# Performance work log

Measured on AMD Instinct MI355X. Metric: run time of the kernel, lower is better.

Reference implementation:

```python
import jax, jax.numpy as jnp
import numpy as np
import math

LS = [0, 1, 2]            # degrees present in all irreps
MAX_L = 2
MULT_IN = 64
MULT_MID = 16
MULT_OUT = 64
N = 20000

# ---- Clebsch-Gordan coefficients in the real spherical-harmonic basis ----

def _f(n):
    return math.factorial(int(n))

def _cg_complex(j1, m1, j2, m2, j3, m3):
    if m1 + m2 != m3:
        return 0.0
    pre = math.sqrt((2 * j3 + 1) * _f(j1 + j2 - j3) * _f(j1 - j2 + j3) * _f(-j1 + j2 + j3) / _f(j1 + j2 + j3 + 1))
    pre *= math.sqrt(_f(j1 + m1) * _f(j1 - m1) * _f(j2 + m2) * _f(j2 - m2) * _f(j3 + m3) * _f(j3 - m3))
    kmin = max(0, j2 - j3 - m1, j1 - j3 + m2)
    kmax = min(j1 + j2 - j3, j1 - m1, j2 + m2)
    s = 0.0
    for k in range(kmin, kmax + 1):
        s += (-1) ** k / (_f(k) * _f(j1 + j2 - j3 - k) * _f(j1 - m1 - k) * _f(j2 + m2 - k) * _f(j3 - j2 + m1 + k) * _f(j3 - j1 - m2 + k))
    return pre * s

def _q(l):
    # complex->real change of basis, rows indexed by real m = -l..l
    Q = np.zeros((2 * l + 1, 2 * l + 1), dtype=complex)
    Q[l, l] = 1.0
    r2 = math.sqrt(2.0)
    for m in range(1, l + 1):
        Q[l + m, l + m] = (-1) ** m / r2
        Q[l + m, l - m] = 1.0 / r2
        Q[l - m, l - m] = 1j / r2
        Q[l - m, l + m] = -1j * (-1) ** m / r2
    return Q

def _real_cg(l1, l2, l3):
    C = np.zeros((2 * l1 + 1, 2 * l2 + 1, 2 * l3 + 1), dtype=complex)
    for m1 in range(-l1, l1 + 1):
        for m2 in range(-l2, l2 + 1):
            m3 = m1 + m2
            if -l3 <= m3 <= l3:
                C[l1 + m1, l2 + m2, l3 + m3] = _cg_complex(l1, m1, l2, m2, l3, m3)
    Q1, Q2, Q3 = _q(l1), _q(l2), _q(l3)
    M = np.einsum('ia,jb,kc,abc->ijk', Q1.conj(), Q2.conj(), Q3, C)
    if np.abs(M.imag).max() > np.abs(M.real).max():
        M = M * (-1j)  # fix parity phase so coefficients are real
    assert np.abs(M.imag).max() < 1e-10
    return np.asarray(M.real, dtype=np.float32)

# triangle-rule paths, truncated at MAX_L
PATHS = [(l1, l2, l) for l1 in LS for l2 in LS for l in range(abs(l1 - l2), min(l1 + l2, MAX_L) + 1)]
CG = {p: jnp.asarray(_real_cg(*p)) for p in PATHS}


def setup_inputs() -> dict:
    key = jax.random.key(0)
    ks = jax.random.split(key, 12)
    inp = {}
    for i, l in enumerate(LS):
        inp[f'x{l}'] = jax.random.normal(ks[i], (N, MULT_IN, 2 * l + 1), dtype=jnp.float32)
    for i, l in enumerate(LS):
        inp[f'W1_{l}'] = jax.random.normal(ks[3 + i], (MULT_IN, MULT_MID), dtype=jnp.float32)
        inp[f'W2_{l}'] = jax.random.normal(ks[6 + i], (MULT_IN, MULT_MID), dtype=jnp.float32)
    tp_mults = {l: sum(MULT_MID * MULT_MID for (l1, l2, lo) in PATHS if lo == l) for l in LS}
    for i, l in enumerate(LS):
        inp[f'W3_{l}'] = jax.random.normal(ks[9 + i], (tp_mults[l], MULT_OUT), dtype=jnp.float32)
    return inp


def _linear(x, W):
    # x: [n, u, i], W: [u, v] -> [n, v, i], normalized like e3nn Linear
    return jnp.einsum('nui,uv->nvi', x, W) / np.float32(math.sqrt(x.shape[1]))


def reference(x0, x1, x2, W1_0, W1_1, W1_2, W2_0, W2_1, W2_2, W3_0, W3_1, W3_2):
    xs = [x0, x1, x2]
    W1 = [W1_0, W1_1, W1_2]
    W2 = [W2_0, W2_1, W2_2]
    W3 = [W3_0, W3_1, W3_2]
    a = [_linear(xs[l], W1[l]) for l in LS]   # branch 1
    b = [_linear(xs[l], W2[l]) for l in LS]   # branch 2
    # CG tensor product up to MAX_L, full (uv) multiplicity
    tp = {l: [] for l in LS}
    n = x0.shape[0]
    for (l1, l2, l) in PATHS:
        t = jnp.einsum('nui,nvj,ijk->nuvk', a[l1], b[l2], CG[(l1, l2, l)])
        tp[l].append(t.reshape(n, MULT_MID * MULT_MID, 2 * l + 1))
    outs = []
    for l in LS:
        z = jnp.concatenate(tp[l], axis=1)        # [n, tp_mult_l, 2l+1]
        y = _linear(z, W3[l])                     # [n, MULT_OUT, 2l+1]
        outs.append(y.reshape(n, -1))
    return jnp.concatenate(outs, axis=1)          # [n, MULT_OUT * 9]
```

## Files before the change

### kernel.cpp

```cpp
#include <hip/hip_runtime.h>


typedef __attribute__((ext_vector_type(4))) float f32x4;
typedef __attribute__((ext_vector_type(4))) float f4;
typedef __attribute__((ext_vector_type(2))) float f2;
typedef __attribute__((ext_vector_type(8))) short short8;
typedef unsigned short ushort_t;
typedef unsigned int uint32;

__device__ __forceinline__ uint32 bfb(float x) {
  uint32 u = __float_as_uint(x);
  return (u + 0x7fffu + ((u >> 16) & 1u)) >> 16;
}

__device__ __forceinline__ uint32 pack2f(f2 z) {
  uint32 lo = __float_as_uint(z.x) + 0x8000u;
  uint32 hi = __float_as_uint(z.y) + 0x8000u;
  return __builtin_amdgcn_perm(hi, lo, 0x07060302u);
}

#define C2   0.7071067811865476f
#define C3   0.5773502691896258f
#define C5   0.4472135954999579f
#define C6   0.4082482904638631f
#define C23  0.8164965809277260f
#define C10  0.3162277660168379f
#define C210 0.6324555320336759f
#define C310 0.5477225575051661f
#define C14  0.2672612419124244f
#define C214 0.5345224838248488f
#define C314 0.4629100498862757f

__global__ __launch_bounds__(256) void pack_w3_kernel(
    const float* __restrict__ W30, const float* __restrict__ W31,
    const float* __restrict__ W32, ushort_t* __restrict__ pack) {
  int lc = blockIdx.x;
  int t = threadIdx.x >> 6;
  int lam = threadIdx.x & 63;
  const float* W;
  int mb;
  float nrm;
  if (lc < 24) {
    W = W30; mb = lc * 32; nrm = 0.036084391824351615f;
  } else if (lc < 72) {
    W = W31; mb = (lc - 24) * 32; nrm = 0.025515518153991442f;
  } else {
    W = W32; mb = (lc - 72) * 32; nrm = 0.025515518153991442f;
  }
  int w = t * 16 + (lam & 15);
  int m0 = mb + (lam >> 4) * 8;
  ushort_t* dst = pack + ((size_t)(lc * 4 + t) * 64 + lam) * 8;
#pragma unroll
  for (int j = 0; j < 8; ++j)
    dst[j] = (ushort_t)bfb(W[(size_t)(m0 + j) * 64 + w] * nrm);
}

template <int NK, int JD, class F>
__device__ __forceinline__ void zgenv(const float* bsj, ushort_t* zrow, F f) {
  uint32 zp[NK][8];
#pragma unroll
  for (int oc = 0; oc < 2; ++oc) {
    f2 bb4[JD][4];
#pragma unroll
    for (int j = 0; j < JD; ++j) {
      f4 lo = *(const f4*)(bsj + j * 16 + oc * 8);
      f4 hi = *(const f4*)(bsj + j * 16 + oc * 8 + 4);
      bb4[j][0] = lo.xy; bb4[j][1] = lo.zw;
      bb4[j][2] = hi.xy; bb4[j][3] = hi.zw;
    }
#pragma unroll
    for (int q = 0; q < 4; ++q) {
      f2 bcol[JD], z[NK];
#pragma unroll
      for (int j = 0; j < JD; ++j) bcol[j] = bb4[j][q];
      f(bcol, z);
#pragma unroll
      for (int k = 0; k < NK; ++k) zp[k][oc * 4 + q] = pack2f(z[k]);
    }
  }
#pragma unroll
  for (int k = 0; k < NK; ++k) {
    uint32* d = (uint32*)(zrow + k * (16 * 264));
    *(uint4*)(d) = make_uint4(zp[k][0], zp[k][1], zp[k][2], zp[k][3]);
    *(uint4*)(d + 4) = make_uint4(zp[k][4], zp[k][5], zp[k][6], zp[k][7]);
  }
}

template <int NROW>
__device__ __forceinline__ void mfma_acc(const ushort_t* zs, const ushort_t* pack,
                                         int kbase, int pcbase, int wt, int lane,
                                         f32x4* acc) {
  int srow = lane & 15, quad = lane >> 4;
  const ushort_t* ab = zs + (kbase * 16 + srow) * 264 + quad * 8;
  const ushort_t* bb = pack + ((size_t)(pcbase * 4 + wt) * 64 + lane) * 8;
#pragma unroll
  for (int c = 0; c < 8; ++c) {
    short8 B = *(const short8*)(bb + (size_t)c * 2048);
#pragma unroll
    for (int rt = 0; rt < NROW; ++rt) {
      short8 A = *(const short8*)(ab + rt * (16 * 264) + c * 32);
      acc[rt] = __builtin_amdgcn_mfma_f32_16x16x32_bf16(A, B, acc[rt], 0, 0, 0);
    }
  }
}

__global__ __launch_bounds__(256, 2) void tdense_kernel(
    const float* __restrict__ x0, const float* __restrict__ x1,
    const float* __restrict__ x2, const float* __restrict__ W10,
    const float* __restrict__ W20, const float* __restrict__ W11,
    const float* __restrict__ W21, const float* __restrict__ W12,
    const float* __restrict__ W22, const ushort_t* __restrict__ pack,
    float* __restrict__ out) {
  __shared__ float b_s[2368];
  __shared__ __align__(16) ushort_t z_s[25344];

  const int tid = threadIdx.x;
  const int nbase = blockIdx.x * 16;
  const int s = tid >> 4, v = tid & 15;

  const int n = nbase + s;
  const float* px0 = x0 + (size_t)n * 64;
  const float* px1 = x1 + (size_t)n * 192;
  const float* px2 = x2 + (size_t)n * 320;
  float a0 = 0.f, a1x = 0.f, a1y = 0.f, a1z = 0.f;
  float a2[5] = {0.f, 0.f, 0.f, 0.f, 0.f};
  float b0 = 0.f, b1x = 0.f, b1y = 0.f, b1z = 0.f;
  float b2[5] = {0.f, 0.f, 0.f, 0.f, 0.f};
  for (int u4 = 0; u4 < 16; ++u4) {
    f4 xv0 = *(const f4*)(px0 + u4 * 4);
    f4 xa = *(const f4*)(px1 + u4 * 12);
    f4 xb = *(const f4*)(px1 + u4 * 12 + 4);
    f4 xc = *(const f4*)(px1 + u4 * 12 + 8);
    f4 ya = *(const f4*)(px2 + u4 * 20);
    f4 yb = *(const f4*)(px2 + u4 * 20 + 4);
    f4 yc = *(const f4*)(px2 + u4 * 20 + 8);
    f4 yd = *(const f4*)(px2 + u4 * 20 + 12);
    f4 ye = *(const f4*)(px2 + u4 * 20 + 16);
    float x1e[12], x2e[20];
#pragma unroll
    for (int e = 0; e < 4; ++e) { x1e[e] = xa[e]; x1e[4 + e] = xb[e]; x1e[8 + e] = xc[e]; }
#pragma unroll
    for (int e = 0; e < 4; ++e) {
      x2e[e] = ya[e]; x2e[4 + e] = yb[e]; x2e[8 + e] = yc[e];
      x2e[12 + e] = yd[e]; x2e[16 + e] = ye[e];
    }
#pragma unroll
    for (int r = 0; r < 4; ++r) {
      int u = u4 * 4 + r;
      float wa0 = W10[u * 16 + v], wb0 = W20[u * 16 + v];
      float wa1 = W11[u * 16 + v], wb1 = W21[u * 16 + v];
      float wa2 = W12[u * 16 + v], wb2 = W22[u * 16 + v];
      float xx = xv0[r];
      a0 += xx * wa0; b0 += xx * wb0;
      float e0 = x1e[r * 3 + 0], e1 = x1e[r * 3 + 1], e2 = x1e[r * 3 + 2];
      a1x += e0 * wa1; a1y += e1 * wa1; a1z += e2 * wa1;
      b1x += e0 * wb1; b1y += e1 * wb1; b1z += e2 * wb1;
#pragma unroll
      for (int j = 0; j < 5; ++j) {
        float ev = x2e[r * 5 + j];
        a2[j] += ev * wa2;
        b2[j] += ev * wb2;
      }
    }
  }
  const float inv8 = 0.125f;
  float ar[9];
  ar[0] = a0 * inv8;
  ar[1] = a1x * inv8; ar[2] = a1y * inv8; ar[3] = a1z * inv8;
#pragma unroll
  for (int j = 0; j < 5; ++j) ar[4 + j] = a2[j] * inv8;
  {
    float* bw = b_s + s * 148 + v;
    bw[0] = b0 * inv8;
    bw[16] = b1x * inv8; bw[32] = b1y * inv8; bw[48] = b1z * inv8;
#pragma unroll
    for (int j = 0; j < 5; ++j) bw[64 + j * 16] = b2[j] * inv8;
  }

  const int lane = tid & 63, wt = tid >> 6;
  f32x4 acc0[1], acc1[3], acc2[5];
  acc0[0] = (f32x4)(0.f);
#pragma unroll
  for (int i = 0; i < 3; ++i) acc1[i] = (f32x4)(0.f);
#pragma unroll
  for (int i = 0; i < 5; ++i) acc2[i] = (f32x4)(0.f);

  __syncthreads();

  const float* bsl0 = b_s + s * 148;
  const float* bsl1 = b_s + s * 148 + 16;
  const float* bsl2 = b_s + s * 148 + 64;
  ushort_t* zr0 = z_s + s * 264 + v * 16;
#define ZROW(kb) (zr0 + (kb) * (16 * 264))

  zgenv<1, 1>(bsl0, ZROW(0), [&](const f2* b, f2* z) { z[0] = ar[0] * b[0]; });
  zgenv<1, 3>(bsl1, ZROW(1), [&](const f2* b, f2* z) {
    z[0] = -C3 * (ar[1] * b[0] + ar[2] * b[1] + ar[3] * b[2]);
  });
  zgenv<1, 5>(bsl2, ZROW(2), [&](const f2* b, f2* z) {
    z[0] = C5 * (ar[4] * b[0] + ar[5] * b[1] + ar[6] * b[2] + ar[7] * b[3] + ar[8] * b[4]);
  });
  zgenv<3, 3>(bsl1, ZROW(3), [&](const f2* b, f2* z) {
    z[0] = ar[0] * b[0]; z[1] = ar[0] * b[1]; z[2] = ar[0] * b[2];
  });
  __syncthreads();
  mfma_acc<1>(z_s, pack, 0, 0, wt, lane, acc0);
  mfma_acc<1>(z_s, pack, 1, 8, wt, lane, acc0);
  mfma_acc<1>(z_s, pack, 2, 16, wt, lane, acc0);
  mfma_acc<3>(z_s, pack, 3, 24, wt, lane, acc1);
  __syncthreads();

  zgenv<3, 1>(bsl0, ZROW(0), [&](const f2* b, f2* z) {
    z[0] = ar[1] * b[0]; z[1] = ar[2] * b[0]; z[2] = ar[3] * b[0];
  });
  zgenv<3, 3>(bsl1, ZROW(3), [&](const f2* b, f2* z) {
    z[0] = C2 * (ar[2] * b[2] - ar[3] * b[1]);
    z[1] = C2 * (ar[3] * b[0] - ar[1] * b[2]);
    z[2] = C2 * (ar[1] * b[1] - ar[2] * b[0]);
  });
  __syncthreads();
  mfma_acc<3>(z_s, pack, 0, 32, wt, lane, acc1);
  mfma_acc<3>(z_s, pack, 3, 40, wt, lane, acc1);
  __syncthreads();

  zgenv<3, 5>(bsl2, ZROW(0), [&](const f2* b, f2* z) {
    z[0] = -C310 * ar[2] * b[1] + C10 * ar[1] * b[2] - C310 * ar[3] * b[0] + C310 * ar[1] * b[4];
    z[1] = -C210 * ar[2] * b[2] - C310 * ar[3] * b[3] - C310 * ar[1] * b[1];
    z[2] = -C310 * ar[2] * b[3] + C10 * ar[3] * b[2] - C310 * ar[1] * b[0] - C310 * ar[3] * b[4];
  });
  zgenv<3, 3>(bsl1, ZROW(3), [&](const f2* b, f2* z) {
    z[0] = -C310 * ar[5] * b[1] + C10 * ar[6] * b[0] - C310 * ar[4] * b[2] + C310 * ar[8] * b[0];
    z[1] = -C210 * ar[6] * b[1] - C310 * ar[7] * b[2] - C310 * ar[5] * b[0];
    z[2] = -C310 * ar[7] * b[1] + C10 * ar[6] * b[2] - C310 * ar[4] * b[0] - C310 * ar[8] * b[2];
  });
  __syncthreads();
  mfma_acc<3>(z_s, pack, 0, 48, wt, lane, acc1);
  mfma_acc<3>(z_s, pack, 3, 56, wt, lane, acc1);
  __syncthreads();

  zgenv<3, 5>(bsl2, ZROW(0), [&](const f2* b, f2* z) {
    z[0] = C10 * (ar[8] * b[3] - ar[7] * b[4] + ar[4] * b[1] - ar[5] * b[0]) +
           C310 * (ar[7] * b[2] - ar[6] * b[3]);
    z[1] = C10 * (ar[5] * b[3] - ar[7] * b[1]) + C210 * (ar[4] * b[4] - ar[8] * b[0]);
    z[2] = C10 * (ar[8] * b[1] - ar[5] * b[4] + ar[7] * b[0] - ar[4] * b[3]) +
           C310 * (ar[6] * b[1] - ar[5] * b[2]);
  });
  __syncthreads();
  mfma_acc<3>(z_s, pack, 0, 64, wt, lane, acc1);
  __syncthreads();

  zgenv<5, 5>(bsl2, ZROW(0), [&](const f2* b, f2* z) {
    z[0] = ar[0] * b[0]; z[1] = ar[0] * b[1]; z[2] = ar[0] * b[2];
    z[3] = ar[0] * b[3]; z[4] = ar[0] * b[4];
  });
  __syncthreads();
  mfma_acc<5>(z_s, pack, 0, 72, wt, lane, acc2);
  __syncthreads();

  zgenv<5, 3>(bsl1, ZROW(0), [&](const f2* b, f2* z) {
    z[0] = C2 * (ar[1] * b[2] + ar[3] * b[0]);
    z[1] = C2 * (ar[2] * b[0] + ar[1] * b[1]);
    z[2] = C23 * ar[2] * b[1] - C6 * (ar[1] * b[0] + ar[3] * b[2]);
    z[3] = C2 * (ar[2] * b[2] + ar[3] * b[1]);
    z[4] = C2 * (ar[3] * b[2] - ar[1] * b[0]);
  });
  __syncthreads();
  mfma_acc<5>(z_s, pack, 0, 80, wt, lane, acc2);
  __syncthreads();

  zgenv<5, 5>(bsl2, ZROW(0), [&](const f2* b, f2* z) {
    z[0] = C23 * ar[2] * b[4] + C6 * ar[1] * b[1] - C6 * ar[3] * b[3];
    z[1] = C6 * ar[2] * b[3] - C6 * ar[1] * b[0] - C2 * ar[3] * b[2] - C6 * ar[3] * b[4];
    z[2] = C2 * (ar[3] * b[1] - ar[1] * b[3]);
    z[3] = -C6 * ar[2] * b[1] + C2 * ar[1] * b[2] + C6 * ar[3] * b[0] - C6 * ar[1] * b[4];
    z[4] = -C23 * ar[2] * b[0] + C6 * ar[1] * b[3] + C6 * ar[3] * b[1];
  });
  __syncthreads();
  mfma_acc<5>(z_s, pack, 0, 88, wt, lane, acc2);
  __syncthreads();

  zgenv<5, 1>(bsl0, ZROW(0), [&](const f2* b, f2* z) {
    z[0] = ar[4] * b[0]; z[1] = ar[5] * b[0]; z[2] = ar[6] * b[0];
    z[3] = ar[7] * b[0]; z[4] = ar[8] * b[0];
  });
  __syncthreads();
  mfma_acc<5>(z_s, pack, 0, 96, wt, lane, acc2);
  __syncthreads();

  zgenv<5, 3>(bsl1, ZROW(0), [&](const f2* b, f2* z) {
    z[0] = -C23 * ar[8] * b[1] - C6 * ar[5] * b[0] + C6 * ar[7] * b[2];
    z[1] = -C6 * ar[7] * b[1] + C6 * ar[4] * b[0] + C2 * ar[6] * b[2] + C6 * ar[8] * b[2];
    z[2] = C2 * (ar[7] * b[0] - ar[5] * b[2]);
    z[3] = C6 * ar[5] * b[1] - C2 * ar[6] * b[0] - C6 * ar[4] * b[2] + C6 * ar[8] * b[0];
    z[4] = C23 * ar[4] * b[1] - C6 * ar[7] * b[0] - C6 * ar[5] * b[2];
  });
  __syncthreads();
  mfma_acc<5>(z_s, pack, 0, 104, wt, lane, acc2);
  __syncthreads();

  zgenv<5, 5>(bsl2, ZROW(0), [&](const f2* b, f2* z) {
    z[0] = C214 * (ar[6] * b[0] + ar[4] * b[2]) - C314 * (ar[5] * b[3] + ar[7] * b[1]);
    z[1] = -C14 * (ar[6] * b[1] + ar[5] * b[2]) + C314 * (ar[5] * b[4] + ar[8] * b[1]) -
           C314 * (ar[7] * b[0] + ar[4] * b[3]);
    z[2] = -C214 * ar[6] * b[2] - C14 * (ar[5] * b[1] + ar[7] * b[3]) +
           C214 * (ar[4] * b[0] + ar[8] * b[4]);
    z[3] = -C14 * (ar[6] * b[3] + ar[7] * b[2]) - C314 * (ar[5] * b[0] + ar[4] * b[1]) -
           C314 * (ar[7] * b[4] + ar[8] * b[3]);
    z[4] = C214 * (ar[6] * b[4] + ar[8] * b[2]) + C314 * (ar[5] * b[1] - ar[7] * b[3]);
  });
  __syncthreads();
  mfma_acc<5>(z_s, pack, 0, 112, wt, lane, acc2);
#undef ZROW

  {
    const int col = lane & 15, quad = lane >> 4;
    const int w = wt * 16 + col;
#pragma unroll
    for (int r = 0; r < 4; ++r) {
      int so = quad * 4 + r;
      float* row = out + (size_t)(nbase + so) * 576;
      row[w] = acc0[0][r];
      row[64 + w * 3 + 0] = acc1[0][r];
      row[64 + w * 3 + 1] = acc1[1][r];
      row[64 + w * 3 + 2] = acc1[2][r];
#pragma unroll
      for (int k = 0; k < 5; ++k) row[256 + w * 5 + k] = acc2[k][r];
    }
  }
}

extern "C" void kernel_launch(void* const* d_in, const int* in_sizes, int n_in,
                              void* d_out, int out_size, void* d_ws, size_t ws_size,
                              hipStream_t stream) {
  const float* x0 = (const float*)d_in[0];
  const float* x1 = (const float*)d_in[1];
  const float* x2 = (const float*)d_in[2];
  const float* W10 = (const float*)d_in[3];
  const float* W20 = (const float*)d_in[4];
  const float* W11 = (const float*)d_in[5];
  const float* W21 = (const float*)d_in[6];
  const float* W12 = (const float*)d_in[7];
  const float* W22 = (const float*)d_in[8];
  const float* W30 = (const float*)d_in[9];
  const float* W31 = (const float*)d_in[10];
  const float* W32 = (const float*)d_in[11];
  ushort_t* pack = (ushort_t*)d_ws;

  hipLaunchKernelGGL(pack_w3_kernel, dim3(120), dim3(256), 0, stream,
                     W30, W31, W32, pack);

  int nsamp = in_sizes[0] / 64;
  int nblocks = nsamp / 16;
  hipLaunchKernelGGL(tdense_kernel, dim3(nblocks), dim3(256), 0, stream,
                     x0, x1, x2, W10, W20, W11, W21, W12, W22, pack,
                     (float*)d_out);
}
```

Before: 222.7 us.

## Double-buffer z tiles and split MFMA work by K-half and column pairs

Splits the shared z staging area into two buffers so the next z tile is generated while MFMAs consume the previous one, and breaks 5-row groups into 3+2 pieces so they fit. Each wave now covers two output column tiles over half the K range (h), sharing each A fragment between two B fragments. A final LDS reduction adds the two K-half partial sums before the store. This trades extra accumulator registers and a reduction step for fewer idle barrier phases and more reuse of A loads.

```diff
diff --git a/kernel.cpp b/kernel.cpp
--- a/kernel.cpp
+++ b/kernel.cpp
@@ -12,7 +12,6 @@
   uint32 u = __float_as_uint(x);
   return (u + 0x7fffu + ((u >> 16) & 1u)) >> 16;
 }
-
 __device__ __forceinline__ uint32 pack2f(f2 z) {
   uint32 lo = __float_as_uint(z.x) + 0x8000u;
   uint32 hi = __float_as_uint(z.y) + 0x8000u;
@@ -87,22 +86,26 @@
 }
 
 template <int NROW>
-__device__ __forceinline__ void mfma_acc(const ushort_t* zs, const ushort_t* pack,
-                                         int kbase, int pcbase, int wt, int lane,
-                                         f32x4* acc) {
-  int srow = lane & 15, quad = lane >> 4;
-  const ushort_t* ab = zs + (kbase * 16 + srow) * 264 + quad * 8;
-  const ushort_t* bb = pack + ((size_t)(pcbase * 4 + wt) * 64 + lane) * 8;
-#pragma unroll
-  for (int c = 0; c < 8; ++c) {
-    short8 B = *(const short8*)(bb + (size_t)c * 2048);
+__device__ __forceinline__ void mfma2(const ushort_t* zb, const ushort_t* pk,
+                                      int pcbase, int h, int wt0, int lane,
+                                      f32x4* accA, f32x4* accB) {
+  const int srow = lane & 15, quad = lane >> 4;
+  const ushort_t* ab = zb + srow * 264 + quad * 8 + h * 128;
+  const ushort_t* bb = pk + ((size_t)((pcbase + h * 4) * 4 + wt0) * 64 + lane) * 8;
+#pragma unroll
+  for (int c = 0; c < 4; ++c) {
+    short8 B0 = *(const short8*)(bb + (size_t)c * 2048);
+    short8 B1 = *(const short8*)(bb + (size_t)c * 2048 + 512);
 #pragma unroll
     for (int rt = 0; rt < NROW; ++rt) {
       short8 A = *(const short8*)(ab + rt * (16 * 264) + c * 32);
-      acc[rt] = __builtin_amdgcn_mfma_f32_16x16x32_bf16(A, B, acc[rt], 0, 0, 0);
-    }
-  }
-}
+      accA[rt] = __builtin_amdgcn_mfma_f32_16x16x32_bf16(A, B0, accA[rt], 0, 0, 0);
+      accB[rt] = __builtin_amdgcn_mfma_f32_16x16x32_bf16(A, B1, accB[rt], 0, 0, 0);
+    }
+  }
+}
+
+#define ZB 12672
 
 __global__ __launch_bounds__(256, 2) void tdense_kernel(
     const float* __restrict__ x0, const float* __restrict__ x1,
@@ -112,7 +115,7 @@
     const float* __restrict__ W22, const ushort_t* __restrict__ pack,
     float* __restrict__ out) {
   __shared__ float b_s[2368];
-  __shared__ __align__(16) ushort_t z_s[25344];
+  __shared__ __align__(16) ushort_t zbuf[2 * ZB];
 
   const int tid = threadIdx.x;
   const int nbase = blockIdx.x * 16;
@@ -177,154 +180,223 @@
     for (int j = 0; j < 5; ++j) bw[64 + j * 16] = b2[j] * inv8;
   }
 
-  const int lane = tid & 63, wt = tid >> 6;
-  f32x4 acc0[1], acc1[3], acc2[5];
-  acc0[0] = (f32x4)(0.f);
-#pragma unroll
-  for (int i = 0; i < 3; ++i) acc1[i] = (f32x4)(0.f);
-#pragma unroll
-  for (int i = 0; i < 5; ++i) acc2[i] = (f32x4)(0.f);
-
-  __syncthreads();
+  const int lane = tid & 63;
+  const int wv = tid >> 6;
+  const int p2 = (wv & 1) * 2;
+  const int h = wv >> 1;
+
+  f32x4 aA0, aB0, aA1[3], aB1[3], aA2[5], aB2[5];
+  aA0 = (f32x4)(0.f); aB0 = (f32x4)(0.f);
+#pragma unroll
+  for (int i = 0; i < 3; ++i) { aA1[i] = (f32x4)(0.f); aB1[i] = (f32x4)(0.f); }
+#pragma unroll
+  for (int i = 0; i < 5; ++i) { aA2[i] = (f32x4)(0.f); aB2[i] = (f32x4)(0.f); }
 
   const float* bsl0 = b_s + s * 148;
-  const float* bsl1 = b_s + s * 148 + 16;
-  const float* bsl2 = b_s + s * 148 + 64;
-  ushort_t* zr0 = z_s + s * 264 + v * 16;
-#define ZROW(kb) (zr0 + (kb) * (16 * 264))
-
-  zgenv<1, 1>(bsl0, ZROW(0), [&](const f2* b, f2* z) { z[0] = ar[0] * b[0]; });
-  zgenv<1, 3>(bsl1, ZROW(1), [&](const f2* b, f2* z) {
+  const float* bsl1 = bsl0 + 16;
+  const float* bsl2 = bsl0 + 64;
+  ushort_t* z0 = zbuf + s * 264 + v * 16;
+  ushort_t* z1 = z0 + ZB;
+  const ushort_t* Zb0 = zbuf;
+  const ushort_t* Zb1 = zbuf + ZB;
+
+  zgenv<1, 1>(bsl0, z0, [&](const f2* b, f2* z) { z[0] = ar[0] * b[0]; });
+  zgenv<1, 3>(bsl1, z0 + 4224, [&](const f2* b, f2* z) {
     z[0] = -C3 * (ar[1] * b[0] + ar[2] * b[1] + ar[3] * b[2]);
   });
-  zgenv<1, 5>(bsl2, ZROW(2), [&](const f2* b, f2* z) {
+  zgenv<1, 5>(bsl2, z0 + 8448, [&](const f2* b, f2* z) {
     z[0] = C5 * (ar[4] * b[0] + ar[5] * b[1] + ar[6] * b[2] + ar[7] * b[3] + ar[8] * b[4]);
   });
-  zgenv<3, 3>(bsl1, ZROW(3), [&](const f2* b, f2* z) {
+  __syncthreads();
+
+  zgenv<3, 3>(bsl1, z1, [&](const f2* b, f2* z) {
     z[0] = ar[0] * b[0]; z[1] = ar[0] * b[1]; z[2] = ar[0] * b[2];
   });
-  __syncthreads();
-  mfma_acc<1>(z_s, pack, 0, 0, wt, lane, acc0);
-  mfma_acc<1>(z_s, pack, 1, 8, wt, lane, acc0);
-  mfma_acc<1>(z_s, pack, 2, 16, wt, lane, acc0);
-  mfma_acc<3>(z_s, pack, 3, 24, wt, lane, acc1);
-  __syncthreads();
-
-  zgenv<3, 1>(bsl0, ZROW(0), [&](const f2* b, f2* z) {
+  mfma2<1>(Zb0, pack, 0, h, p2, lane, &aA0, &aB0);
+  mfma2<1>(Zb0 + 4224, pack, 8, h, p2, lane, &aA0, &aB0);
+  mfma2<1>(Zb0 + 8448, pack, 16, h, p2, lane, &aA0, &aB0);
+  __syncthreads();
+
+  zgenv<3, 1>(bsl0, z0, [&](const f2* b, f2* z) {
     z[0] = ar[1] * b[0]; z[1] = ar[2] * b[0]; z[2] = ar[3] * b[0];
   });
-  zgenv<3, 3>(bsl1, ZROW(3), [&](const f2* b, f2* z) {
+  mfma2<3>(Zb1, pack, 24, h, p2, lane, aA1, aB1);
+  __syncthreads();
+
+  zgenv<3, 3>(bsl1, z1, [&](const f2* b, f2* z) {
     z[0] = C2 * (ar[2] * b[2] - ar[3] * b[1]);
     z[1] = C2 * (ar[3] * b[0] - ar[1] * b[2]);
     z[2] = C2 * (ar[1] * b[1] - ar[2] * b[0]);
   });
-  __syncthreads();
-  mfma_acc<3>(z_s, pack, 0, 32, wt, lane, acc1);
-  mfma_acc<3>(z_s, pack, 3, 40, wt, lane, acc1);
-  __syncthreads();
-
-  zgenv<3, 5>(bsl2, ZROW(0), [&](const f2* b, f2* z) {
+  mfma2<3>(Zb0, pack, 32, h, p2, lane, aA1, aB1);
+  __syncthreads();
+
+  zgenv<3, 5>(bsl2, z0, [&](const f2* b, f2* z) {
     z[0] = -C310 * ar[2] * b[1] + C10 * ar[1] * b[2] - C310 * ar[3] * b[0] + C310 * ar[1] * b[4];
     z[1] = -C210 * ar[2] * b[2] - C310 * ar[3] * b[3] - C310 * ar[1] * b[1];
     z[2] = -C310 * ar[2] * b[3] + C10 * ar[3] * b[2] - C310 * ar[1] * b[0] - C310 * ar[3] * b[4];
   });
-  zgenv<3, 3>(bsl1, ZROW(3), [&](const f2* b, f2* z) {
+  mfma2<3>(Zb1, pack, 40, h, p2, lane, aA1, aB1);
+  __syncthreads();
+
+  zgenv<3, 3>(bsl1, z1, [&](const f2* b, f2* z) {
     z[0] = -C310 * ar[5] * b[1] + C10 * ar[6] * b[0] - C310 * ar[4] * b[2] + C310 * ar[8] * b[0];
     z[1] = -C210 * ar[6] * b[1] - C310 * ar[7] * b[2] - C310 * ar[5] * b[0];
     z[2] = -C310 * ar[7] * b[1] + C10 * ar[6] * b[2] - C310 * ar[4] * b[0] - C310 * ar[8] * b[2];
   });
-  __syncthreads();
-  mfma_acc<3>(z_s, pack, 0, 48, wt, lane, acc1);
-  mfma_acc<3>(z_s, pack, 3, 56, wt, lane, acc1);
-  __syncthreads();
-
-  zgenv<3, 5>(bsl2, ZROW(0), [&](const f2* b, f2* z) {
+  mfma2<3>(Zb0, pack, 48, h, p2, lane, aA1, aB1);
+  __syncthreads();
+
+  zgenv<3, 5>(bsl2, z0, [&](const f2* b, f2* z) {
     z[0] = C10 * (ar[8] * b[3] - ar[7] * b[4] + ar[4] * b[1] - ar[5] * b[0]) +
            C310 * (ar[7] * b[2] - ar[6] * b[3]);
     z[1] = C10 * (ar[5] * b[3] - ar[7] * b[1]) + C210 * (ar[4] * b[4] - ar[8] * b[0]);
     z[2] = C10 * (ar[8] * b[1] - ar[5] * b[4] + ar[7] * b[0] - ar[4] * b[3]) +
            C310 * (ar[6] * b[1] - ar[5] * b[2]);
   });
-  __syncthreads();
-  mfma_acc<3>(z_s, pack, 0, 64, wt, lane, acc1);
-  __syncthreads();
-
-  zgenv<5, 5>(bsl2, ZROW(0), [&](const f2* b, f2* z) {
+  mfma2<3>(Zb1, pack, 56, h, p2, lane, aA1, aB1);
+  __syncthreads();
+
+  zgenv<3, 5>(bsl2, z1, [&](const f2* b, f2* z) {
     z[0] = ar[0] * b[0]; z[1] = ar[0] * b[1]; z[2] = ar[0] * b[2];
-    z[3] = ar[0] * b[3]; z[4] = ar[0] * b[4];
-  });
-  __syncthreads();
-  mfma_acc<5>(z_s, pack, 0, 72, wt, lane, acc2);
-  __syncthreads();
-
-  zgenv<5, 3>(bsl1, ZROW(0), [&](const f2* b, f2* z) {
+  });
+  mfma2<3>(Zb0, pack, 64, h, p2, lane, aA1, aB1);
+  __syncthreads();
+
+  zgenv<2, 5>(bsl2, z0, [&](const f2* b, f2* z) {
+    z[0] = ar[0] * b[3]; z[1] = ar[0] * b[4];
+  });
+  mfma2<3>(Zb1, pack, 72, h, p2, lane, aA2, aB2);
+  __syncthreads();
+
+  zgenv<3, 3>(bsl1, z1, [&](const f2* b, f2* z) {
     z[0] = C2 * (ar[1] * b[2] + ar[3] * b[0]);
     z[1] = C2 * (ar[2] * b[0] + ar[1] * b[1]);
     z[2] = C23 * ar[2] * b[1] - C6 * (ar[1] * b[0] + ar[3] * b[2]);
-    z[3] = C2 * (ar[2] * b[2] + ar[3] * b[1]);
-    z[4] = C2 * (ar[3] * b[2] - ar[1] * b[0]);
-  });
-  __syncthreads();
-  mfma_acc<5>(z_s, pack, 0, 80, wt, lane, acc2);
-  __syncthreads();
-
-  zgenv<5, 5>(bsl2, ZROW(0), [&](const f2* b, f2* z) {
+  });
+  mfma2<2>(Zb0, pack, 72, h, p2, lane, aA2 + 3, aB2 + 3);
+  __syncthreads();
+
+  zgenv<2, 3>(bsl1, z0, [&](const f2* b, f2* z) {
+    z[0] = C2 * (ar[2] * b[2] + ar[3] * b[1]);
+    z[1] = C2 * (ar[3] * b[2] - ar[1] * b[0]);
+  });
+  mfma2<3>(Zb1, pack, 80, h, p2, lane, aA2, aB2);
+  __syncthreads();
+
+  zgenv<3, 5>(bsl2, z1, [&](const f2* b, f2* z) {
     z[0] = C23 * ar[2] * b[4] + C6 * ar[1] * b[1] - C6 * ar[3] * b[3];
     z[1] = C6 * ar[2] * b[3] - C6 * ar[1] * b[0] - C2 * ar[3] * b[2] - C6 * ar[3] * b[4];
     z[2] = C2 * (ar[3] * b[1] - ar[1] * b[3]);
-    z[3] = -C6 * ar[2] * b[1] + C2 * ar[1] * b[2] + C6 * ar[3] * b[0] - C6 * ar[1] * b[4];
-    z[4] = -C23 * ar[2] * b[0] + C6 * ar[1] * b[3] + C6 * ar[3] * b[1];
-  });
-  __syncthreads();
-  mfma_acc<5>(z_s, pack, 0, 88, wt, lane, acc2);
-  __syncthreads();
-
-  zgenv<5, 1>(bsl0, ZROW(0), [&](const f2* b, f2* z) {
+  });
+  mfma2<2>(Zb0, pack, 80, h, p2, lane, aA2 + 3, aB2 + 3);
+  __syncthreads();
+
+  zgenv<2, 5>(bsl2, z0, [&](const f2* b, f2* z) {
+    z[0] = -C6 * ar[2] * b[1] + C2 * ar[1] * b[2] + C6 * ar[3] * b[0] - C6 * ar[1] * b[4];
+    z[1] = -C23 * ar[2] * b[0] + C6 * ar[1] * b[3] + C6 * ar[3] * b[1];
+  });
+  mfma2<3>(Zb1, pack, 88, h, p2, lane, aA2, aB2);
+  __syncthreads();
+
+  zgenv<3, 1>(bsl0, z1, [&](const f2* b, f2* z) {
     z[0] = ar[4] * b[0]; z[1] = ar[5] * b[0]; z[2] = ar[6] * b[0];
-    z[3] = ar[7] * b[0]; z[4] = ar[8] * b[0];
-  });
-  __syncthreads();
-  mfma_acc<5>(z_s, pack, 0, 96, wt, lane, acc2);
-  __syncthreads();
-
-  zgenv<5, 3>(bsl1, ZROW(0), [&](const f2* b, f2* z) {
+  });
+  mfma2<2>(Zb0, pack, 88, h, p2, lane, aA2 + 3, aB2 + 3);
+  __syncthreads();
+
+  zgenv<2, 1>(bsl0, z0, [&](const f2* b, f2* z) {
+    z[0] = ar[7] * b[0]; z[1] = ar[8] * b[0];
+  });
+  mfma2<3>(Zb1, pack, 96, h, p2, lane, aA2, aB2);
+  __syncthreads();
+
+  zgenv<3, 3>(bsl1, z1, [&](const f2* b, f2* z) {
     z[0] = -C23 * ar[8] * b[1] - C6 * ar[5] * b[0] + C6 * ar[7] * b[2];
     z[1] = -C6 * ar[7] * b[1] + C6 * ar[4] * b[0] + C2 * ar[6] * b[2] + C6 * ar[8] * b[2];
     z[2] = C2 * (ar[7] * b[0] - ar[5] * b[2]);
-    z[3] = C6 * ar[5] * b[1] - C2 * ar[6] * b[0] - C6 * ar[4] * b[2] + C6 * ar[8] * b[0];
-    z[4] = C23 * ar[4] * b[1] - C6 * ar[7] * b[0] - C6 * ar[5] * b[2];
-  });
-  __syncthreads();
-  mfma_acc<5>(z_s, pack, 0, 104, wt, lane, acc2);
-  __syncthreads();
-
-  zgenv<5, 5>(bsl2, ZROW(0), [&](const f2* b, f2* z) {
+  });
+  mfma2<2>(Zb0, pack, 96, h, p2, lane, aA2 + 3, aB2 + 3);
+  __syncthreads();
+
+  zgenv<2, 3>(bsl1, z0, [&](const f2* b, f2* z) {
+    z[0] = C6 * ar[5] * b[1] - C2 * ar[6] * b[0] - C6 * ar[4] * b[2] + C6 * ar[8] * b[0];
+    z[1] = C23 * ar[4] * b[1] - C6 * ar[7] * b[0] - C6 * ar[5] * b[2];
+  });
+  mfma2<3>(Zb1, pack, 104, h, p2, lane, aA2, aB2);
+  __syncthreads();
+
+  zgenv<3, 5>(bsl2, z1, [&](const f2* b, f2* z) {
     z[0] = C214 * (ar[6] * b[0] + ar[4] * b[2]) - C314 * (ar[5] * b[3] + ar[7] * b[1]);
     z[1] = -C14 * (ar[6] * b[1] + ar[5] * b[2]) + C314 * (ar[5] * b[4] + ar[8] * b[1]) -
            C314 * (ar[7] * b[0] + ar[4] * b[3]);
     z[2] = -C214 * ar[6] * b[2] - C14 * (ar[5] * b[1] + ar[7] * b[3]) +
            C214 * (ar[4] * b[0] + ar[8] * b[4]);
-    z[3] = -C14 * (ar[6] * b[3] + ar[7] * b[2]) - C314 * (ar[5] * b[0] + ar[4] * b[1]) -
+  });
+  mfma2<2>(Zb0, pack, 104, h, p2, lane, aA2 + 3, aB2 + 3);
+  __syncthreads();
+
+  zgenv<2, 5>(bsl2, z0, [&](const f2* b, f2* z) {
+    z[0] = -C14 * (ar[6] * b[3] + ar[7] * b[2]) - C314 * (ar[5] * b[0] + ar[4] * b[1]) -
            C314 * (ar[7] * b[4] + ar[8] * b[3]);
-    z[4] = C214 * (ar[6] * b[4] + ar[8] * b[2]) + C314 * (ar[5] * b[1] - ar[7] * b[3]);
-  });
-  __syncthreads();
-  mfma_acc<5>(z_s, pack, 0, 112, wt, lane, acc2);
-#undef ZROW
-
-  {
-    const int col = lane & 15, quad = lane >> 4;
-    const int w = wt * 16 + col;
+    z[1] = C214 * (ar[6] * b[4] + ar[8] * b[2]) + C314 * (ar[5] * b[1] - ar[7] * b[3]);
+  });
+  mfma2<3>(Zb1, pack, 112, h, p2, lane, aA2, aB2);
+  __syncthreads();
+
+  mfma2<2>(Zb0, pack, 112, h, p2, lane, aA2 + 3, aB2 + 3);
+  __syncthreads();
+
+  float* red = (float*)zbuf;
+  const int col = lane & 15, quad = lane >> 4;
+  if (h == 0) {
+#pragma unroll
+    for (int pp = 0; pp < 2; ++pp) {
+      int wt = p2 + pp;
+      const f32x4* src0 = pp ? &aB0 : &aA0;
+      const f32x4* src1 = pp ? aB1 : aA1;
+      const f32x4* src2 = pp ? aB2 : aA2;
+      *(f4*)(red + (wt * 9 + 0) * 256 + lane * 4) = src0[0];
+#pragma unroll
+      for (int o = 0; o < 3; ++o)
+        *(f4*)(red + (wt * 9 + 1 + o) * 256 + lane * 4) = src1[o];
+#pragma unroll
+      for (int o = 0; o < 5; ++o)
+        *(f4*)(red + (wt * 9 + 4 + o) * 256 + lane * 4) = src2[o];
+    }
+  }
+  __syncthreads();
+  if (h == 1) {
+    aA0 += *(const f4*)(red + (p2 * 9 + 0) * 256 + lane * 4);
+    aB0 += *(const f4*)(red + ((p2 + 1) * 9 + 0) * 256 + lane * 4);
+#pragma unroll
+    for (int o = 0; o < 3; ++o) {
+      aA1[o] += *(const f4*)(red + (p2 * 9 + 1 + o) * 256 + lane * 4);
+      aB1[o] += *(const f4*)(red + ((p2 + 1) * 9 + 1 + o) * 256 + lane * 4);
+    }
+#pragma unroll
+    for (int o = 0; o < 5; ++o) {
+      aA2[o] += *(const f4*)(red + (p2 * 9 + 4 + o) * 256 + lane * 4);
+      aB2[o] += *(const f4*)(red + ((p2 + 1) * 9 + 4 + o) * 256 + lane * 4);
+    }
+    const int w0 = p2 * 16 + col, w1 = w0 + 16;
 #pragma unroll
     for (int r = 0; r < 4; ++r) {
       int so = quad * 4 + r;
       float* row = out + (size_t)(nbase + so) * 576;
-      row[w] = acc0[0][r];
-      row[64 + w * 3 + 0] = acc1[0][r];
-      row[64 + w * 3 + 1] = acc1[1][r];
-      row[64 + w * 3 + 2] = acc1[2][r];
-#pragma unroll
-      for (int k = 0; k < 5; ++k) row[256 + w * 5 + k] = acc2[k][r];
+      row[w0] = aA0[r];
+      row[w1] = aB0[r];
+      row[64 + w0 * 3 + 0] = aA1[0][r];
+      row[64 + w0 * 3 + 1] = aA1[1][r];
+      row[64 + w0 * 3 + 2] = aA1[2][r];
+      row[64 + w1 * 3 + 0] = aB1[0][r];
+      row[64 + w1 * 3 + 1] = aB1[1][r];
+      row[64 + w1 * 3 + 2] = aB1[2][r];
+#pragma unroll
+      for (int k = 0; k < 5; ++k) {
+        row[256 + w0 * 5 + k] = aA2[k][r];
+        row[256 + w1 * 5 + k] = aB2[k][r];
+      }
     }
   }
 }
```

New measurement: 218.9 us. Within noise of the previous version (-1.7%).
